# Optimization experiments

Measured on AMD Instinct MI355X. Metric: run time of the kernel, lower is better.

Reference implementation:

```python
import jax, jax.numpy as jnp
import numpy as np

DIM = 2048
N_HEADS = 16
HEAD_DIM = 128
EPS = 1e-6


def setup_inputs() -> dict:
    key = jax.random.key(0)
    ks = jax.random.split(key, 8)
    b, gf, gh, gw = 1, 8, 16, 24
    s = gf * gh * gw
    c = HEAD_DIM // 2
    w = lambda k: 0.02 * jax.random.normal(k, (DIM, DIM), jnp.float32)
    return {
        "x": jax.random.normal(ks[0], (b, s, DIM), jnp.float32),
        "freqs_angle": jax.random.normal(ks[1], (1024, c), jnp.float32),
        "Wq": w(ks[2]), "bq": jnp.zeros((DIM,), jnp.float32),
        "Wk": w(ks[3]), "bk": jnp.zeros((DIM,), jnp.float32),
        "Wv": w(ks[4]), "bv": jnp.zeros((DIM,), jnp.float32),
        "Wo": w(ks[5]), "bo": jnp.zeros((DIM,), jnp.float32),
        "gq": jnp.ones((DIM,), jnp.float32),
        "gk": jnp.ones((DIM,), jnp.float32),
        "seq_len": s, "grid_f": gf, "grid_h": gh, "grid_w": gw,
    }


def _rms(t, g):
    return t * jax.lax.rsqrt(jnp.mean(t * t, axis=-1, keepdims=True) + EPS) * g


def _grid_angles(freqs_angle, gf, gh, gw, c):
    # band split [c - 2*(c//3), c//3, c//3] as in rope_apply
    cf = c - 2 * (c // 3)
    ch = cw = c // 3
    af = freqs_angle[:gf, :cf]            # [F, cf]
    ah = freqs_angle[:gh, cf:cf + ch]     # [H, ch]
    aw = freqs_angle[:gw, cf + ch:c]      # [W, cw]
    ang = jnp.concatenate([
        jnp.broadcast_to(af[:, None, None, :], (gf, gh, gw, cf)),
        jnp.broadcast_to(ah[None, :, None, :], (gf, gh, gw, ch)),
        jnp.broadcast_to(aw[None, None, :, :], (gf, gh, gw, cw)),
    ], axis=-1)
    return ang.reshape(gf * gh * gw, c)   # [s, c]


def reference(x, freqs_angle, Wq, bq, Wk, bk, Wv, bv, Wo, bo, gq, gk,
              seq_len, grid_f, grid_h, grid_w):
    b, s, _ = x.shape
    n, d = N_HEADS, HEAD_DIM
    c = d // 2
    ang = _grid_angles(freqs_angle, grid_f, grid_h, grid_w, c)
    cos = jnp.cos(ang)[None, :, None, :]  # [1, s, 1, c]
    sin = jnp.sin(ang)[None, :, None, :]

    def rope(t):  # complex multiply on (even, odd) = (real, imag) pairs
        te, to = t[..., 0::2], t[..., 1::2]
        return jnp.stack([te * cos - to * sin, te * sin + to * cos], axis=-1).reshape(t.shape)

    q = _rms(x @ Wq.T + bq, gq).reshape(b, s, n, d)
    k = _rms(x @ Wk.T + bk, gk).reshape(b, s, n, d)
    v = (x @ Wv.T + bv).reshape(b, s, n, d)
    q, k = rope(q), rope(k)

    scale = np.float32(1.0 / np.sqrt(d))
    scores = jnp.einsum('bqnd,bknd->bnqk', q, k) * scale
    p = jax.nn.softmax(scores, axis=-1)
    o = jnp.einsum('bnqk,bknd->bqnd', p, v).reshape(b, s, n * d)
    return o @ Wo.T + bo
```

## Files before the change

### kernel.cpp

```cpp
#include <hip/hip_runtime.h>
#include <stdint.h>
#include <stddef.h>

typedef __bf16 bf16_t;
typedef __bf16 bf16x8 __attribute__((ext_vector_type(8)));
typedef __bf16 bf16x4 __attribute__((ext_vector_type(4)));
typedef __bf16 bf16x2 __attribute__((ext_vector_type(2)));
typedef float  f32x4  __attribute__((ext_vector_type(4)));
typedef float  f32x16 __attribute__((ext_vector_type(16)));

#define SEQ   3072
#define DIMD  2048
#define NH    16
#define HD    128
#define QKVN  6144

__device__ __forceinline__ void async16(const bf16_t* g, bf16_t* l) {
  __builtin_amdgcn_global_load_lds((const __attribute__((address_space(1))) uint32_t*)g,
                                   (__attribute__((address_space(3))) uint32_t*)l, 16, 0, 0);
}

__global__ __launch_bounds__(256) void cvt_all(const float* __restrict__ x,
                                               const float* __restrict__ Wq,
                                               const float* __restrict__ Wk,
                                               const float* __restrict__ Wv,
                                               const float* __restrict__ Wo,
                                               const float* __restrict__ bq,
                                               const float* __restrict__ bk,
                                               const float* __restrict__ bv,
                                               bf16_t* __restrict__ xb,
                                               bf16_t* __restrict__ Wqkvb,
                                               bf16_t* __restrict__ Wob,
                                               float* __restrict__ bqkv) {
  const int b = blockIdx.x;
  const float* src; bf16_t* dst; int off;
  if (b < 3072)       { src = x;  dst = xb;              off = b; }
  else if (b < 5120)  { src = Wq; dst = Wqkvb;           off = b - 3072; }
  else if (b < 7168)  { src = Wk; dst = Wqkvb + 4194304; off = b - 5120; }
  else if (b < 9216)  { src = Wv; dst = Wqkvb + 8388608; off = b - 7168; }
  else if (b < 11264) { src = Wo; dst = Wob;             off = b - 9216; }
  else {
    int t = (b - 11264) * 256 + threadIdx.x;
    float v;
    if (t < 2048)      v = bq[t];
    else if (t < 4096) v = bk[t - 2048];
    else               v = bv[t - 4096];
    bqkv[t] = v;
    return;
  }
  const int idx = (off * 256 + threadIdx.x) * 8;
  const float4 a = *(const float4*)(src + idx);
  const float4 c = *(const float4*)(src + idx + 4);
  bf16x8 o;
  o[0] = (bf16_t)a.x; o[1] = (bf16_t)a.y; o[2] = (bf16_t)a.z; o[3] = (bf16_t)a.w;
  o[4] = (bf16_t)c.x; o[5] = (bf16_t)c.y; o[6] = (bf16_t)c.z; o[7] = (bf16_t)c.w;
  *(bf16x8*)(dst + idx) = o;
}

template<bool OUT_BF16>
__global__ __launch_bounds__(256, 3) void gemm_nt(const bf16_t* __restrict__ A,
                                                  const bf16_t* __restrict__ B,
                                                  const float* __restrict__ bias,
                                                  void* __restrict__ Cout,
                                                  int M, int N, int K, int PN) {
  __shared__ __align__(16) bf16_t As[128 * 64];
  __shared__ __align__(16) bf16_t Bs[128 * 64];
  const int t = threadIdx.x;
  const int lane = t & 63, wave = t >> 6;
  const int quad = lane >> 4, l15 = lane & 15;
  const int wy = wave >> 1, wx = wave & 1;
  const int f = blockIdx.x;
  const int xcd = f & 7, local = f >> 3;
  const int mblk = local / PN, nblk = xcd * PN + local % PN;
  const size_t bm = (size_t)mblk * 128, bn = (size_t)nblk * 128;
  const bf16_t* Ab = A + bm * K;
  const bf16_t* Bb = B + bn * K;
  f32x4 acc[4][4] = {};
  int srow[4], scol[4];
#pragma unroll
  for (int r = 0; r < 4; r++) {
    int L = r * 256 + t;
    int row = L >> 3, cp = L & 7;
    srow[r] = row;
    scol[r] = (cp ^ (row & 7)) * 8;
  }
  for (int k0 = 0; k0 < K; k0 += 64) {
    __syncthreads();
#pragma unroll
    for (int r = 0; r < 4; r++)
      async16(Ab + (size_t)srow[r] * K + k0 + scol[r], &As[(r * 256 + t) * 8]);
#pragma unroll
    for (int r = 0; r < 4; r++)
      async16(Bb + (size_t)srow[r] * K + k0 + scol[r], &Bs[(r * 256 + t) * 8]);
    __syncthreads();
#pragma unroll
    for (int ks = 0; ks < 2; ks++) {
      bf16x8 af[4], bfv[4];
#pragma unroll
      for (int i = 0; i < 4; i++) {
        int row = wy * 64 + i * 16 + l15;
        af[i] = *(const bf16x8*)&As[row * 64 + (((ks * 4 + quad) ^ (row & 7)) * 8)];
      }
#pragma unroll
      for (int j = 0; j < 4; j++) {
        int row = wx * 64 + j * 16 + l15;
        bfv[j] = *(const bf16x8*)&Bs[row * 64 + (((ks * 4 + quad) ^ (row & 7)) * 8)];
      }
#pragma unroll
      for (int i = 0; i < 4; i++)
#pragma unroll
        for (int j = 0; j < 4; j++)
          acc[i][j] = __builtin_amdgcn_mfma_f32_16x16x32_bf16(af[i], bfv[j], acc[i][j], 0, 0, 0);
    }
  }
#pragma unroll
  for (int i = 0; i < 4; i++) {
#pragma unroll
    for (int j = 0; j < 4; j++) {
      size_t row = bm + wy * 64 + i * 16 + quad * 4;
      size_t col = bn + wx * 64 + j * 16 + l15;
      float bb = bias[col];
#pragma unroll
      for (int r = 0; r < 4; r++) {
        float v = acc[i][j][r] + bb;
        if (OUT_BF16) ((bf16_t*)Cout)[(row + r) * N + col] = (bf16_t)v;
        else          ((float*)Cout)[(row + r) * N + col] = v;
      }
    }
  }
}

__global__ __launch_bounds__(256) void prep(bf16_t* __restrict__ qkv,
                                            bf16_t* __restrict__ pk,
                                            bf16_t* __restrict__ pvt,
                                            const float* __restrict__ gq,
                                            const float* __restrict__ gk,
                                            const float* __restrict__ freqs) {
  __shared__ bf16_t tile[128][65];
  __shared__ float red[2][4];
  const int t = threadIdx.x;
  if (blockIdx.x < 3072) {
    const int s = blockIdx.x;
    bf16_t* row = qkv + (size_t)s * QKVN;
    bf16x8 qv = *(const bf16x8*)&row[t * 8];
    bf16x8 kv = *(const bf16x8*)&row[2048 + t * 8];
    float qf[8], kf[8];
    float qs = 0.f, ks2 = 0.f;
#pragma unroll
    for (int i = 0; i < 8; i++) {
      qf[i] = (float)qv[i]; qs  += qf[i] * qf[i];
      kf[i] = (float)kv[i]; ks2 += kf[i] * kf[i];
    }
#pragma unroll
    for (int m = 1; m < 64; m <<= 1) {
      qs  += __shfl_xor(qs, m);
      ks2 += __shfl_xor(ks2, m);
    }
    const int wave = t >> 6, lane = t & 63;
    if (lane == 0) { red[0][wave] = qs; red[1][wave] = ks2; }
    __syncthreads();
    qs  = red[0][0] + red[0][1] + red[0][2] + red[0][3];
    ks2 = red[1][0] + red[1][1] + red[1][2] + red[1][3];
    const float qsc = rsqrtf(qs  / 2048.f + 1e-6f) * 0.12751745f;
    const float ksc = rsqrtf(ks2 / 2048.f + 1e-6f);
    const int sf = s / 384, rem = s - sf * 384;
    const int sh = rem / 24, sw = rem - sh * 24;
    bf16x8 qo, ko;
#pragma unroll
    for (int u = 0; u < 4; u++) {
      const int col = t * 8 + 2 * u;
      const int i = (col >> 1) & 63;
      const int frow = (i < 22) ? sf : ((i < 43) ? sh : sw);
      const float ang = freqs[frow * 64 + i];
      float sn, cs;
      __sincosf(ang, &sn, &cs);
      float te = qf[2 * u]     * qsc * gq[col];
      float to = qf[2 * u + 1] * qsc * gq[col + 1];
      qo[2 * u]     = (bf16_t)(te * cs - to * sn);
      qo[2 * u + 1] = (bf16_t)(te * sn + to * cs);
      te = kf[2 * u]     * ksc * gk[col];
      to = kf[2 * u + 1] * ksc * gk[col + 1];
      ko[2 * u]     = (bf16_t)(te * cs - to * sn);
      ko[2 * u + 1] = (bf16_t)(te * sn + to * cs);
    }
    *(bf16x8*)&row[t * 8] = qo;
    *(bf16x8*)&pk[((size_t)(t >> 4) * SEQ + s) * HD + (t & 15) * 8] = ko;
  } else {
    const int idx = blockIdx.x - 3072;
    const int h = idx / 48;
    const int s0 = (idx - h * 48) * 64;
#pragma unroll
    for (int r = 0; r < 4; r++) {
      int L = r * 256 + t, s = L >> 4, cp = L & 15;
      bf16x8 v = *(const bf16x8*)&qkv[(size_t)(s0 + s) * QKVN + 4096 + h * HD + cp * 8];
#pragma unroll
      for (int i = 0; i < 8; i++) tile[cp * 8 + i][s] = v[i];
    }
    __syncthreads();
#pragma unroll
    for (int r = 0; r < 4; r++) {
      int L = r * 256 + t, d = L >> 3, c = L & 7;
      bf16x8 o;
#pragma unroll
      for (int i = 0; i < 8; i++) o[i] = tile[d][c * 8 + i];
      *(bf16x8*)&pvt[((size_t)h * HD + d) * SEQ + s0 + c * 8] = o;
    }
  }
}

#define STAGE_KV(BUF, KV1) do {                                              \
    _Pragma("unroll")                                                        \
    for (int r = 0; r < 5; r++) {                                            \
      int L = r * 192 + t;                                                   \
      async16(pkh + (size_t)(KV1) * HD + koff[r], &Ks[BUF][L * 8]);          \
      async16(pvh + (KV1) + voff[r], &Vt[BUF][L * 8]);                       \
    }                                                                        \
    if (t < 64) {                                                            \
      int L = 5 * 192 + t;                                                   \
      async16(pkh + (size_t)(KV1) * HD + koff[5], &Ks[BUF][L * 8]);          \
      async16(pvh + (KV1) + voff[5], &Vt[BUF][L * 8]);                       \
    }                                                                        \
  } while (0)

__global__ __launch_bounds__(192, 2) void flash_attn(const bf16_t* __restrict__ qkv,
                                                     const bf16_t* __restrict__ pk,
                                                     const bf16_t* __restrict__ pvt,
                                                     bf16_t* __restrict__ ob) {
  __shared__ __align__(16) bf16_t Ks[2][64 * 128];
  __shared__ __align__(16) bf16_t Vt[2][128 * 64];
  const int f = blockIdx.x;
  const int wg = (f & 7) * 64 + (f >> 3);
  const int hh = wg >> 5, qt = wg & 31;
  const int s0 = qt * 96;
  const int t = threadIdx.x, wave = t >> 6, lane = t & 63;
  const int l31 = lane & 31, hl = lane >> 5;
  const int wq = wave * 32;
  const bf16_t* pkh = pk  + (size_t)hh * (SEQ * HD);
  const bf16_t* pvh = pvt + (size_t)hh * (HD * SEQ);
  int koff[6], voff[6];
#pragma unroll
  for (int r = 0; r < 6; r++) {
    int L = r * 192 + t;
    int krow = L >> 4, kc = (L & 15) ^ (krow & 7);
    koff[r] = krow * HD + kc * 8;
    int vd = L >> 3, vc = (L & 7) ^ (vd & 7);
    voff[r] = vd * SEQ + vc * 8;
  }
  bf16x8 qfr[8];
#pragma unroll
  for (int ks = 0; ks < 8; ks++)
    qfr[ks] = *(const bf16x8*)&qkv[(size_t)(s0 + wq + l31) * QKVN + hh * HD + ks * 16 + hl * 8];
  bf16x8 vones;
#pragma unroll
  for (int i = 0; i < 8; i++) vones[i] = (bf16_t)1.0f;
  f32x16 oacc[4] = {};
  f32x16 lacc = {};
  STAGE_KV(0, 0);
  for (int kt = 0; kt < SEQ / 64; kt++) {
    const int cur = kt & 1;
    __syncthreads();
    if (kt + 1 < SEQ / 64) STAGE_KV(cur ^ 1, (kt + 1) * 64);
    f32x16 st0 = {}, st1 = {};
    __builtin_amdgcn_s_setprio(1);
#pragma unroll
    for (int ks = 0; ks < 8; ks++) {
      const int r1 = 32 + l31;
      bf16x8 k0 = *(const bf16x8*)&Ks[cur][l31 * 128 + (((ks * 2 + hl) ^ (l31 & 7)) * 8)];
      bf16x8 k1 = *(const bf16x8*)&Ks[cur][r1 * 128 + (((ks * 2 + hl) ^ (r1 & 7)) * 8)];
      st0 = __builtin_amdgcn_mfma_f32_32x32x16_bf16(k0, qfr[ks], st0, 0, 0, 0);
      st1 = __builtin_amdgcn_mfma_f32_32x32x16_bf16(k1, qfr[ks], st1, 0, 0, 0);
    }
    __builtin_amdgcn_s_setprio(0);
    uint32_t c0[8], c1[8];
#pragma unroll
    for (int m = 0; m < 8; m++) {
      bf16x2 w0, w1;
      w0[0] = (bf16_t)__builtin_amdgcn_exp2f(st0[2 * m]);
      w0[1] = (bf16_t)__builtin_amdgcn_exp2f(st0[2 * m + 1]);
      w1[0] = (bf16_t)__builtin_amdgcn_exp2f(st1[2 * m]);
      w1[1] = (bf16_t)__builtin_amdgcn_exp2f(st1[2 * m + 1]);
      c0[m] = __builtin_bit_cast(uint32_t, w0);
      c1[m] = __builtin_bit_cast(uint32_t, w1);
    }
    union U8 { uint32_t u[4]; bf16x8 v; } afr0, afr1, afr2, afr3;
#define BUILD_AFR(DST, CB, B) do {                                           \
      uint32_t sA = hl ? CB[(B) + 0] : CB[(B) + 2];                          \
      uint32_t sB = hl ? CB[(B) + 1] : CB[(B) + 3];                          \
      uint32_t rA = (uint32_t)__shfl_xor((int)sA, 32);                       \
      uint32_t rB = (uint32_t)__shfl_xor((int)sB, 32);                       \
      DST.u[0] = hl ? rA : CB[(B) + 0];                                      \
      DST.u[1] = hl ? rB : CB[(B) + 1];                                      \
      DST.u[2] = hl ? CB[(B) + 2] : rA;                                      \
      DST.u[3] = hl ? CB[(B) + 3] : rB;                                      \
    } while (0)
    BUILD_AFR(afr0, c0, 0);
    BUILD_AFR(afr1, c0, 4);
    BUILD_AFR(afr2, c1, 0);
    BUILD_AFR(afr3, c1, 4);
#undef BUILD_AFR
    __builtin_amdgcn_s_setprio(1);
#define PV_STEP(AFR, S) do {                                                            \
      lacc = __builtin_amdgcn_mfma_f32_32x32x16_bf16(AFR.v, vones, lacc, 0, 0, 0);      \
      _Pragma("unroll")                                                                 \
      for (int dj = 0; dj < 4; dj++) {                                                  \
        const int row = dj * 32 + l31;                                                  \
        bf16x8 vf = *(const bf16x8*)&Vt[cur][row * 64 + ((((S) * 2 + hl) ^ (row & 7)) * 8)]; \
        oacc[dj] = __builtin_amdgcn_mfma_f32_32x32x16_bf16(AFR.v, vf, oacc[dj], 0, 0, 0);    \
      }                                                                                 \
    } while (0)
    PV_STEP(afr0, 0);
    PV_STEP(afr1, 1);
    PV_STEP(afr2, 2);
    PV_STEP(afr3, 3);
#undef PV_STEP
    __builtin_amdgcn_s_setprio(0);
  }
#pragma unroll
  for (int r = 0; r < 16; r++) {
    const float li = 1.f / lacc[r];
    const size_t row = (size_t)(s0 + wq + (r & 3) + 8 * (r >> 2) + 4 * hl);
#pragma unroll
    for (int dj = 0; dj < 4; dj++)
      ob[row * DIMD + hh * HD + dj * 32 + l31] = (bf16_t)(oacc[dj][r] * li);
  }
}

extern "C" void kernel_launch(void* const* d_in, const int* in_sizes, int n_in,
                              void* d_out, int out_size, void* d_ws, size_t ws_size,
                              hipStream_t stream) {
  (void)in_sizes; (void)n_in; (void)out_size;
  const float* x     = (const float*)d_in[0];
  const float* freqs = (const float*)d_in[1];
  const float* Wq    = (const float*)d_in[2];
  const float* bq    = (const float*)d_in[3];
  const float* Wk    = (const float*)d_in[4];
  const float* bk    = (const float*)d_in[5];
  const float* Wv    = (const float*)d_in[6];
  const float* bv    = (const float*)d_in[7];
  const float* Wo    = (const float*)d_in[8];
  const float* bo    = (const float*)d_in[9];
  const float* gq    = (const float*)d_in[10];
  const float* gk    = (const float*)d_in[11];

  char* w = (char*)d_ws;
  bf16_t* xb    = (bf16_t*)(w);
  bf16_t* Wqkvb = (bf16_t*)(w + 12582912);
  bf16_t* Wob   = (bf16_t*)(w + 37748736);
  bf16_t* qkvb  = (bf16_t*)(w + 46137344);
  bf16_t* obuf  = (bf16_t*)(w + 83886080);
  float*  bqkv  = (float*) (w + 96468992);
  bf16_t* pk    = (bf16_t*)(w);
  bf16_t* pvt   = (bf16_t*)(w + 12582912);
  if (ws_size < (size_t)96493568) return;

  cvt_all<<<11288, 256, 0, stream>>>(x, Wq, Wk, Wv, Wo, bq, bk, bv, xb, Wqkvb, Wob, bqkv);

  gemm_nt<true><<<dim3(1152), 256, 0, stream>>>(xb, Wqkvb, bqkv, qkvb, SEQ, QKVN, DIMD, 6);
  prep<<<3840, 256, 0, stream>>>(qkvb, pk, pvt, gq, gk, freqs);
  flash_attn<<<dim3(512), 192, 0, stream>>>(qkvb, pk, pvt, obuf);
  gemm_nt<false><<<dim3(384), 256, 0, stream>>>(obuf, Wob, bo, (float*)d_out, SEQ, DIMD, DIMD, 2);
}
```

Measured before the change: 394.3 us.

## Double-buffer LDS tiles in the bf16 GEMM to overlap loads with MFMA

The GEMM kernel now keeps two LDS buffers for the A and B tiles. It issues the async global-to-LDS loads for the next K tile before running the MFMAs on the current tile, so it needs only one barrier per iteration instead of two. The goal is to hide global load latency behind the matrix math. In exchange LDS use per block doubles to 64 KB and the launch-bounds occupancy hint drops from 3 to 2 blocks per CU, which may reduce latency hiding across blocks.

```diff
diff --git a/kernel.cpp b/kernel.cpp
--- a/kernel.cpp
+++ b/kernel.cpp
@@ -58,13 +58,13 @@
 }
 
 template<bool OUT_BF16>
-__global__ __launch_bounds__(256, 3) void gemm_nt(const bf16_t* __restrict__ A,
+__global__ __launch_bounds__(256, 2) void gemm_nt(const bf16_t* __restrict__ A,
                                                   const bf16_t* __restrict__ B,
                                                   const float* __restrict__ bias,
                                                   void* __restrict__ Cout,
                                                   int M, int N, int K, int PN) {
-  __shared__ __align__(16) bf16_t As[128 * 64];
-  __shared__ __align__(16) bf16_t Bs[128 * 64];
+  __shared__ __align__(16) bf16_t As[2][128 * 64];
+  __shared__ __align__(16) bf16_t Bs[2][128 * 64];
   const int t = threadIdx.x;
   const int lane = t & 63, wave = t >> 6;
   const int quad = lane >> 4, l15 = lane & 15;
@@ -84,27 +84,32 @@
     srow[r] = row;
     scol[r] = (cp ^ (row & 7)) * 8;
   }
-  for (int k0 = 0; k0 < K; k0 += 64) {
+#define G_STAGE(BUF, K0) do {                                                   \
+    _Pragma("unroll")                                                           \
+    for (int r = 0; r < 4; r++)                                                 \
+      async16(Ab + (size_t)srow[r] * K + (K0) + scol[r], &As[BUF][(r * 256 + t) * 8]); \
+    _Pragma("unroll")                                                           \
+    for (int r = 0; r < 4; r++)                                                 \
+      async16(Bb + (size_t)srow[r] * K + (K0) + scol[r], &Bs[BUF][(r * 256 + t) * 8]); \
+  } while (0)
+  const int nk = K >> 6;
+  G_STAGE(0, 0);
+  for (int kt = 0; kt < nk; kt++) {
+    const int cur = kt & 1;
     __syncthreads();
-#pragma unroll
-    for (int r = 0; r < 4; r++)
-      async16(Ab + (size_t)srow[r] * K + k0 + scol[r], &As[(r * 256 + t) * 8]);
-#pragma unroll
-    for (int r = 0; r < 4; r++)
-      async16(Bb + (size_t)srow[r] * K + k0 + scol[r], &Bs[(r * 256 + t) * 8]);
-    __syncthreads();
+    if (kt + 1 < nk) G_STAGE(cur ^ 1, (kt + 1) * 64);
 #pragma unroll
     for (int ks = 0; ks < 2; ks++) {
       bf16x8 af[4], bfv[4];
 #pragma unroll
       for (int i = 0; i < 4; i++) {
         int row = wy * 64 + i * 16 + l15;
-        af[i] = *(const bf16x8*)&As[row * 64 + (((ks * 4 + quad) ^ (row & 7)) * 8)];
+        af[i] = *(const bf16x8*)&As[cur][row * 64 + (((ks * 4 + quad) ^ (row & 7)) * 8)];
       }
 #pragma unroll
       for (int j = 0; j < 4; j++) {
         int row = wx * 64 + j * 16 + l15;
-        bfv[j] = *(const bf16x8*)&Bs[row * 64 + (((ks * 4 + quad) ^ (row & 7)) * 8)];
+        bfv[j] = *(const bf16x8*)&Bs[cur][row * 64 + (((ks * 4 + quad) ^ (row & 7)) * 8)];
       }
 #pragma unroll
       for (int i = 0; i < 4; i++)
@@ -113,6 +118,7 @@
           acc[i][j] = __builtin_amdgcn_mfma_f32_16x16x32_bf16(af[i], bfv[j], acc[i][j], 0, 0, 0);
     }
   }
+#undef G_STAGE
 #pragma unroll
   for (int i = 0; i < 4; i++) {
 #pragma unroll
```

Result: no change. 401.3 us (+1.8%).
